# Kernel optimization log

Hardware: AMD Instinct MI355X
Metric: run time of the kernel (lower is better)

The kernel has to match this reference:

```python
import jax, jax.numpy as jnp
import numpy as np

B, T_DEC, T_ENC = 64, 128, 256
D_X, N_HIDDEN, N_FEED = 1024, 1024, 1024


def _glorot(key, shape):
    fan_in = shape[0]
    return jax.random.normal(key, shape, dtype=jnp.float32) / np.sqrt(fan_in)


def setup_inputs() -> dict:
    key = jax.random.key(0)
    ks = jax.random.split(key, 10)
    H = N_HIDDEN
    return {
        "x": jax.random.normal(ks[0], (B, T_DEC, D_X), dtype=jnp.float32),
        "o_enc": jax.random.normal(ks[1], (B, T_ENC, H), dtype=jnp.float32),
        "h_enc": jax.random.normal(ks[2], (B, H), dtype=jnp.float32),
        # input-feeding FFN: Dense(n_feed, tanh), input dim = n_hidden
        "Wfeed": _glorot(ks[3], (H, N_FEED)),
        "bfeed": jnp.zeros((N_FEED,), dtype=jnp.float32),
        # GRU (keras v2, reset_after=True): kernel [n_feed+d_x, 3H], recurrent [H, 3H]
        "Wx": _glorot(ks[4], (N_FEED + D_X, 3 * H)),
        "Wh": _glorot(ks[5], (H, 3 * H)),
        "bxi": jnp.zeros((3 * H,), dtype=jnp.float32),  # input bias
        "bhr": jnp.zeros((3 * H,), dtype=jnp.float32),  # recurrent bias (reset_after)
        # attention FFN: Dense(n_hidden, tanh), input dim = 2H (concat[value, h_dec])
        "Watt": _glorot(ks[6], (2 * H, H)),
        "batt": jnp.zeros((H,), dtype=jnp.float32),
    }


def reference(x, o_enc, h_enc, Wfeed, bfeed, Wx, Wh, bxi, bhr, Watt, batt):
    # x: [B, T_dec, d_x], o_enc: [B, T_enc, H], h_enc: [B, H]
    def step(carry, x_t):
        h, i_feed = carry  # h: [B,H] GRU state, i_feed: [B,H] previous attention output
        # input feeding FFN + concat with current token
        i_cat = jnp.concatenate([jnp.tanh(i_feed @ Wfeed + bfeed), x_t], axis=-1)
        # GRU cell (keras reset_after=True semantics)
        gx = i_cat @ Wx + bxi  # [B, 3H]
        gh = h @ Wh + bhr      # [B, 3H]
        xz, xr, xh = jnp.split(gx, 3, axis=-1)
        hz, hr, hh = jnp.split(gh, 3, axis=-1)
        z = jax.nn.sigmoid(xz + hz)
        r = jax.nn.sigmoid(xr + hr)
        hcand = jnp.tanh(xh + r * hh)
        h_new = z * h + (1.0 - z) * hcand  # [B, H]
        # Luong dot attention over encoder outputs
        scores = jnp.einsum('bh,bth->bt', h_new, o_enc)       # [B, T_enc]
        attn = jax.nn.softmax(scores, axis=-1)
        value = jnp.einsum('bt,bth->bh', attn, o_enc)         # [B, H]
        h_att = jnp.tanh(jnp.concatenate([value, h_new], axis=-1) @ Watt + batt)
        return (h_new, h_att), h_att

    i_feed0 = jnp.zeros_like(h_enc)
    x_t_major = jnp.swapaxes(x, 0, 1)  # [T_dec, B, d_x]
    _, outs = jax.lax.scan(step, (h_enc, i_feed0), x_t_major)
    return jnp.swapaxes(outs, 0, 1)  # [B, T_dec, H]
```

## Files before the change

### kernel.cpp

```cpp
#include <hip/hip_runtime.h>
#include <hip/hip_bf16.h>


#define NWG 256
#define NTHR 1024
constexpr int BB = 64, TD = 128, TE = 256, HH = 1024, H3 = 3072;

typedef __attribute__((ext_vector_type(8))) __bf16 bf16x8;
typedef __attribute__((ext_vector_type(4))) float f32x4;
using bf = __hip_bfloat16;

__device__ __forceinline__ f32x4 mfma16(bf16x8 a, bf16x8 b, f32x4 c) {
  return __builtin_amdgcn_mfma_f32_16x16x32_bf16(a, b, c, 0, 0, 0);
}

struct Args {
  const float *x, *o_enc, *bfeed, *bxi, *bhr, *batt;
  const bf *Wf0, *Wf1, *Wf2, *Wh0, *Wh1, *Wh2;
  const bf *WxF0, *WxF1, *WxF2, *WxX0, *WxX1, *WxX2, *Wa0, *Wa1, *Wa2;
  float *h_f32;
  float *gx;
  float *gh, *scores;
  bf *hs0, *hs1, *hs2, *ff0, *ff1, *ff2, *ifd0, *ifd1, *ifd2;
  bf *xt0, *xt1, *xt2, *vl0, *vl1, *vl2;
  unsigned *cnt, *cnt2, *go, *afl;
  float *out;
};

__device__ __forceinline__ void gbar(unsigned ep, const Args& a, int wg) {
  __syncthreads();
  if (threadIdx.x == 0) {
    __threadfence();
    unsigned* sub = a.cnt + (wg & 15) * 32;
    unsigned o = __hip_atomic_fetch_add(sub, 1u, __ATOMIC_ACQ_REL, __HIP_MEMORY_SCOPE_AGENT);
    if (o == 15) {
      __hip_atomic_store(sub, 0u, __ATOMIC_RELAXED, __HIP_MEMORY_SCOPE_AGENT);
      unsigned o2 = __hip_atomic_fetch_add(a.cnt2, 1u, __ATOMIC_ACQ_REL, __HIP_MEMORY_SCOPE_AGENT);
      if (o2 == 15) {
        __hip_atomic_store(a.cnt2, 0u, __ATOMIC_RELAXED, __HIP_MEMORY_SCOPE_AGENT);
        __hip_atomic_store(a.go, ep, __ATOMIC_RELEASE, __HIP_MEMORY_SCOPE_AGENT);
      }
    }
    while (__hip_atomic_load(a.go, __ATOMIC_RELAXED, __HIP_MEMORY_SCOPE_AGENT) < ep)
      __builtin_amdgcn_s_sleep(2);
    __threadfence();
  }
  __syncthreads();
}

__device__ __forceinline__ void split3_write(bf* p0, bf* p1, bf* p2, size_t i, float v) {
  bf b0 = __float2bfloat16(v);
  float r1 = v - __bfloat162float(b0);
  bf b1 = __float2bfloat16(r1);
  float r2 = r1 - __bfloat162float(b1);
  p0[i] = b0; p1[i] = b1; p2[i] = __float2bfloat16(r2);
}

template <int K>
__device__ __forceinline__ f32x4 gemm6(const bf* A0, const bf* A1, const bf* A2,
                                       const bf* B0, const bf* B1, const bf* B2) {
  f32x4 c0 = {0.f, 0.f, 0.f, 0.f}, c1 = c0, c2 = c0, c3 = c0;
#pragma unroll 4
  for (int k = 0; k < K; k += 32) {
    bf16x8 a0 = *(const bf16x8*)(A0 + k);
    bf16x8 a1 = *(const bf16x8*)(A1 + k);
    bf16x8 a2 = *(const bf16x8*)(A2 + k);
    bf16x8 b0 = *(const bf16x8*)(B0 + k);
    bf16x8 b1 = *(const bf16x8*)(B1 + k);
    bf16x8 b2 = *(const bf16x8*)(B2 + k);
    c0 = mfma16(a0, b0, c0);
    c1 = mfma16(a0, b1, c1);
    c2 = mfma16(a1, b0, c2);
    c3 = mfma16(a1, b1, c3);
    c0 = mfma16(a0, b2, c0);
    c1 = mfma16(a2, b0, c1);
  }
  f32x4 s;
#pragma unroll
  for (int i = 0; i < 4; ++i) s[i] = (c0[i] + c1[i]) + (c2[i] + c3[i]);
  return s;
}

__global__ __launch_bounds__(NTHR, 4) void decoder_main(Args a) {
  const int wg = blockIdx.x;
  const int tid = threadIdx.x;
  const int lane = tid & 63;
  const int wv = tid >> 6;
  const int lrow = lane & 15;
  const int lkg = lane >> 4;

  __shared__ float s_u[4096];
  __shared__ float s_h[HH];
  __shared__ float s_sm[TE];
  __shared__ float s_red[8];
  __shared__ float s_val[2][256];
  __shared__ int s_idx[TE];
  __shared__ int s_wcnt[4];

  unsigned ep = 0;

  for (int t = 0; t < TD; ++t) {
    {
      const bool isf = (wg < 64);
      const int j0 = (isf ? wg : wg - 64) * 16;
      const bf* A0 = isf ? a.ifd0 : a.hs0;
      const bf* A1 = isf ? a.ifd1 : a.hs1;
      const bf* A2 = isf ? a.ifd2 : a.hs2;
      const bf* B0 = isf ? a.Wf0 : a.Wh0;
      const bf* B1 = isf ? a.Wf1 : a.Wh1;
      const bf* B2 = isf ? a.Wf2 : a.Wh2;
      const int mt = wv >> 2, kq = wv & 3;
      const size_t aoff = (size_t)(mt * 16 + lrow) * HH + kq * 256 + lkg * 8;
      const size_t boff = (size_t)(j0 + lrow) * HH + kq * 256 + lkg * 8;
      f32x4 acc = gemm6<256>(A0 + aoff, A1 + aoff, A2 + aoff, B0 + boff, B1 + boff, B2 + boff);
#pragma unroll
      for (int r = 0; r < 4; ++r) s_u[kq * 1024 + mt * 256 + (lkg * 4 + r) * 16 + lrow] = acc[r];
      __syncthreads();
      {
        const int row = tid >> 4, c = tid & 15;
        const int emt = row >> 4, r2 = row & 15;
        const int e = emt * 256 + r2 * 16 + c;
        float v = (s_u[e] + s_u[1024 + e]) + (s_u[2048 + e] + s_u[3072 + e]);
        const int col = j0 + c;
        if (isf) {
          float f = tanhf(v + a.bfeed[col]);
          split3_write(a.ff0, a.ff1, a.ff2, (size_t)row * HH + col, f);
        } else {
          a.gh[(size_t)row * H3 + col] = v + a.bhr[col];
        }
      }
    }
    gbar(++ep, a, wg);

    {
      const int jt = wg >> 2, sub = wg & 3;
      if (wv < 12) {
        const int ci = wv >> 2, ku = wv & 3;
        const int c2 = sub * 3 + ci;
        const int g = c2 >> 2, mt = c2 & 3;
        const int op = ku >> 1, kh = ku & 1;
        const bf* A0 = op ? a.xt0 : a.ff0;
        const bf* A1 = op ? a.xt1 : a.ff1;
        const bf* A2 = op ? a.xt2 : a.ff2;
        const bf* B0 = op ? a.WxX0 : a.WxF0;
        const bf* B1 = op ? a.WxX1 : a.WxF1;
        const bf* B2 = op ? a.WxX2 : a.WxF2;
        const size_t aoff = (size_t)(mt * 16 + lrow) * HH + kh * 512 + lkg * 8;
        const size_t boff = (size_t)(g * HH + jt * 16 + lrow) * HH + kh * 512 + lkg * 8;
        f32x4 acc = gemm6<512>(A0 + aoff, A1 + aoff, A2 + aoff, B0 + boff, B1 + boff, B2 + boff);
#pragma unroll
        for (int r = 0; r < 4; ++r)
          s_u[ci * 1024 + ku * 256 + (lkg * 4 + r) * 16 + lrow] = acc[r];
      }
      __syncthreads();
      if (tid < 768) {
        const int ci2 = tid >> 8, e = tid & 255;
        const int r16 = e >> 4, c16 = e & 15;
        const int base = ci2 * 1024 + e;
        float v = (s_u[base] + s_u[base + 256]) + (s_u[base + 512] + s_u[base + 768]);
        const int c2 = sub * 3 + ci2;
        const int g = c2 >> 2, mt = c2 & 3;
        a.gx[(size_t)(mt * 16 + r16) * H3 + g * 1024 + jt * 16 + c16] = v;
      }
    }
    gbar(++ep, a, wg);

    {
      const int b = wg >> 2, q = wg & 3;
      const float* hold = a.h_f32 + (size_t)(t & 1) * (BB * HH);
      float* hnew = a.h_f32 + (size_t)((t + 1) & 1) * (BB * HH);
      const float* ghb = a.gh + (size_t)b * H3;
      {
        const int col = tid;
        const float* gxb = a.gx + (size_t)b * H3;
        float gz = a.bxi[col] + gxb[col];
        float gr = a.bxi[HH + col] + gxb[HH + col];
        float gc = a.bxi[2 * HH + col] + gxb[2 * HH + col];
        float z = 1.f / (1.f + expf(-(gz + ghb[col])));
        float rr = 1.f / (1.f + expf(-(gr + ghb[HH + col])));
        float hc = tanhf(gc + rr * ghb[2 * HH + col]);
        float hn = z * hold[(size_t)b * HH + col] + (1.f - z) * hc;
        s_h[col] = hn;
        if (q == 0) {
          hnew[(size_t)b * HH + col] = hn;
          split3_write(a.hs0, a.hs1, a.hs2, (size_t)b * HH + col, hn);
        }
      }
      __syncthreads();
      {
        f32x4 sh0 = *(const f32x4*)(s_h + 0 + lane * 4);
        f32x4 sh1 = *(const f32x4*)(s_h + 256 + lane * 4);
        f32x4 sh2 = *(const f32x4*)(s_h + 512 + lane * 4);
        f32x4 sh3 = *(const f32x4*)(s_h + 768 + lane * 4);
        const float* obase = a.o_enc + ((size_t)b * TE + q * 64 + wv * 4) * HH + lane * 4;
        f32x4 o0 = *(const f32x4*)(obase);
        f32x4 o1 = *(const f32x4*)(obase + 256);
        f32x4 o2 = *(const f32x4*)(obase + 512);
        f32x4 o3 = *(const f32x4*)(obase + 768);
#pragma unroll
        for (int i = 0; i < 4; ++i) {
          f32x4 n0, n1, n2, n3;
          if (i + 1 < 4) {
            const float* nr = obase + (size_t)(i + 1) * HH;
            n0 = *(const f32x4*)(nr);
            n1 = *(const f32x4*)(nr + 256);
            n2 = *(const f32x4*)(nr + 512);
            n3 = *(const f32x4*)(nr + 768);
          }
          float s = o0[0] * sh0[0] + o0[1] * sh0[1] + o0[2] * sh0[2] + o0[3] * sh0[3]
                  + o1[0] * sh1[0] + o1[1] * sh1[1] + o1[2] * sh1[2] + o1[3] * sh1[3]
                  + o2[0] * sh2[0] + o2[1] * sh2[1] + o2[2] * sh2[2] + o2[3] * sh2[3]
                  + o3[0] * sh3[0] + o3[1] * sh3[1] + o3[2] * sh3[2] + o3[3] * sh3[3];
          for (int off = 32; off; off >>= 1) s += __shfl_xor(s, off);
          if (lane == 0) a.scores[(size_t)b * TE + q * 64 + wv * 4 + i] = s;
          o0 = n0; o1 = n1; o2 = n2; o3 = n3;
        }
      }
      __syncthreads();
      if (tid == 0) {
        __threadfence();
        __hip_atomic_store(&a.afl[b * 4 + q], (unsigned)(t + 1),
                           __ATOMIC_RELEASE, __HIP_MEMORY_SCOPE_AGENT);
        for (int p = 1; p < 4; ++p) {
          unsigned idx = b * 4 + ((q + p) & 3);
          while (__hip_atomic_load(&a.afl[idx], __ATOMIC_RELAXED, __HIP_MEMORY_SCOPE_AGENT)
                 < (unsigned)(t + 1))
            __builtin_amdgcn_s_sleep(1);
        }
        __threadfence();
      }
      __syncthreads();
      float sc = 0.f, p = 0.f;
      if (tid < 256) {
        sc = a.scores[(size_t)b * TE + tid];
        float v = sc;
        for (int off = 32; off; off >>= 1) v = fmaxf(v, __shfl_xor(v, off));
        if (lane == 0) s_red[wv] = v;
      }
      __syncthreads();
      {
        float mx = fmaxf(fmaxf(s_red[0], s_red[1]), fmaxf(s_red[2], s_red[3]));
        if (tid < 256) {
          p = expf(sc - mx);
          float sum = p;
          for (int off = 32; off; off >>= 1) sum += __shfl_xor(sum, off);
          if (lane == 0) s_red[4 + wv] = sum;
        }
      }
      __syncthreads();
      bool act = false;
      unsigned long long bm = 0;
      if (tid < 256) {
        float tot = s_red[4] + s_red[5] + s_red[6] + s_red[7];
        float w2 = p / tot;
        s_sm[tid] = w2;
        act = (w2 > 1e-8f);
        bm = __ballot(act);
        if (lane == 0) s_wcnt[wv] = __popcll(bm);
      }
      __syncthreads();
      if (tid < 256 && act) {
        int base = 0;
        for (int w2i = 0; w2i < wv; ++w2i) base += s_wcnt[w2i];
        int pos = base + __popcll(bm & ((1ULL << lane) - 1));
        s_idx[pos] = tid;
      }
      __syncthreads();
      const int nact = s_wcnt[0] + s_wcnt[1] + s_wcnt[2] + s_wcnt[3];
      if (tid < 512) {
        const int c = tid & 255, th = tid >> 8;
        const int j = q * 256 + c;
        const float* ob = a.o_enc + (size_t)b * TE * HH + j;
        float accv = 0.f;
        for (int ii = th; ii < nact; ii += 2) {
          const int tt2 = s_idx[ii];
          accv += s_sm[tt2] * ob[(size_t)tt2 * HH];
        }
        s_val[th][c] = accv;
      }
      __syncthreads();
      if (tid < 256)
        split3_write(a.vl0, a.vl1, a.vl2, (size_t)b * HH + q * 256 + tid,
                     s_val[0][tid] + s_val[1][tid]);
    }
    gbar(++ep, a, wg);

    {
      const int cu = wg & 63;
      const int mt = wg >> 6;
      const int kq16 = wv;
      const bool isv = (kq16 < 8);
      const int koff = (kq16 & 7) * 128;
      const bf* A0 = isv ? a.vl0 : a.hs0;
      const bf* A1 = isv ? a.vl1 : a.hs1;
      const bf* A2 = isv ? a.vl2 : a.hs2;
      const size_t aoff = (size_t)(mt * 16 + lrow) * HH + koff + lkg * 8;
      const size_t boff = (size_t)(cu * 16 + lrow) * 2048 + kq16 * 128 + lkg * 8;
      f32x4 acc = gemm6<128>(A0 + aoff, A1 + aoff, A2 + aoff,
                             a.Wa0 + boff, a.Wa1 + boff, a.Wa2 + boff);
#pragma unroll
      for (int r = 0; r < 4; ++r)
        s_u[kq16 * 256 + (lkg * 4 + r) * 16 + lrow] = acc[r];
      __syncthreads();
      if (tid < 256) {
        const int r16 = tid >> 4, c16 = tid & 15;
        const int e = r16 * 16 + c16;
        float v = a.batt[cu * 16 + c16];
#pragma unroll
        for (int kq = 0; kq < 16; ++kq) v += s_u[kq * 256 + e];
        float hv = tanhf(v);
        const int row = mt * 16 + r16;
        const int col = cu * 16 + c16;
        a.out[((size_t)row * TD + t) * HH + col] = hv;
        split3_write(a.ifd0, a.ifd1, a.ifd2, (size_t)row * HH + col, hv);
      }
      if (wg < 64 && t + 1 < TD) {
        split3_write(a.xt0, a.xt1, a.xt2, (size_t)wg * HH + tid,
                     a.x[((size_t)wg * TD + (t + 1)) * HH + tid]);
      }
    }
    gbar(++ep, a, wg);
  }
}

__global__ void k_tr3(const float* src, bf* d0, bf* d1, bf* d2, int R, int C) {
  __shared__ float tile[32][33];
  int c0 = blockIdx.x * 32, r0 = blockIdx.y * 32;
  int tx = threadIdx.x & 31, ty = threadIdx.x >> 5;
  for (int i = ty; i < 32; i += 8)
    tile[i][tx] = src[(size_t)(r0 + i) * C + c0 + tx];
  __syncthreads();
  for (int i = ty; i < 32; i += 8) {
    float v = tile[tx][i];
    size_t o = (size_t)(c0 + i) * R + r0 + tx;
    bf b0 = __float2bfloat16(v);
    float r1 = v - __bfloat162float(b0);
    bf b1 = __float2bfloat16(r1);
    d0[o] = b0; d1[o] = b1; d2[o] = __float2bfloat16(r1 - __bfloat162float(b1));
  }
}

__global__ void k_init(const float* h_enc, float* h_f32, bf* h0, bf* h1, bf* h2,
                       bf* i0, bf* i1, bf* i2, const float* x, bf* x0, bf* x1, bf* x2) {
  int i = blockIdx.x * blockDim.x + threadIdx.x;
  float v = h_enc[i];
  h_f32[i] = v;
  split3_write(h0, h1, h2, i, v);
  bf z = __float2bfloat16(0.f);
  i0[i] = z; i1[i] = z; i2[i] = z;
  int row = i >> 10, col = i & 1023;
  split3_write(x0, x1, x2, i, x[((size_t)row * TD + 0) * HH + col]);
}

extern "C" void kernel_launch(void* const* d_in, const int* in_sizes, int n_in,
                              void* d_out, int out_size, void* d_ws, size_t ws_size,
                              hipStream_t stream) {
  const float* x     = (const float*)d_in[0];
  const float* o_enc = (const float*)d_in[1];
  const float* h_enc = (const float*)d_in[2];
  const float* Wfeed = (const float*)d_in[3];
  const float* bfeed = (const float*)d_in[4];
  const float* Wx    = (const float*)d_in[5];
  const float* Wh    = (const float*)d_in[6];
  const float* bxi   = (const float*)d_in[7];
  const float* bhr   = (const float*)d_in[8];
  const float* Watt  = (const float*)d_in[9];
  const float* batt  = (const float*)d_in[10];

  char* w = (char*)d_ws;
  auto alloc = [&](size_t b) { char* p = w; w += (b + 255) & ~255ULL; return p; };

  const size_t M1 = (size_t)1024 * 1024 * 2;
  bf* Wf[3];  for (auto& p : Wf)  p = (bf*)alloc(M1);
  bf* Wh_[3]; for (auto& p : Wh_) p = (bf*)alloc(3 * M1);
  bf* WxF[3]; for (auto& p : WxF) p = (bf*)alloc(3 * M1);
  bf* WxX[3]; for (auto& p : WxX) p = (bf*)alloc(3 * M1);
  bf* Wa[3];  for (auto& p : Wa)  p = (bf*)alloc(2 * M1);
  float* h_f32  = (float*)alloc((size_t)2 * BB * HH * 4);
  float* gx     = (float*)alloc((size_t)BB * H3 * 4);
  float* gh     = (float*)alloc((size_t)BB * H3 * 4);
  float* scores = (float*)alloc((size_t)BB * TE * 4);
  const size_t AB = (size_t)BB * HH * 2;
  bf *hs[3], *ff[3], *ifd[3], *xt[3], *vl[3];
  for (auto& p : hs)  p = (bf*)alloc(AB);
  for (auto& p : ff)  p = (bf*)alloc(AB);
  for (auto& p : ifd) p = (bf*)alloc(AB);
  for (auto& p : xt)  p = (bf*)alloc(AB);
  for (auto& p : vl)  p = (bf*)alloc(AB);
  unsigned* flags = (unsigned*)alloc(8192);

  hipMemsetAsync(flags, 0, 8192, stream);
  k_tr3<<<dim3(32, 32), 256, 0, stream>>>(Wfeed, Wf[0], Wf[1], Wf[2], 1024, 1024);
  k_tr3<<<dim3(96, 32), 256, 0, stream>>>(Wx, WxF[0], WxF[1], WxF[2], 1024, 3072);
  k_tr3<<<dim3(96, 32), 256, 0, stream>>>(Wx + (size_t)1024 * 3072, WxX[0], WxX[1], WxX[2], 1024, 3072);
  k_tr3<<<dim3(96, 32), 256, 0, stream>>>(Wh, Wh_[0], Wh_[1], Wh_[2], 1024, 3072);
  k_tr3<<<dim3(32, 64), 256, 0, stream>>>(Watt, Wa[0], Wa[1], Wa[2], 2048, 1024);
  k_init<<<BB * HH / 256, 256, 0, stream>>>(h_enc, h_f32, hs[0], hs[1], hs[2],
                                            ifd[0], ifd[1], ifd[2], x, xt[0], xt[1], xt[2]);

  Args a;
  a.x = x; a.o_enc = o_enc; a.bfeed = bfeed; a.bxi = bxi; a.bhr = bhr; a.batt = batt;
  a.Wf0 = Wf[0]; a.Wf1 = Wf[1]; a.Wf2 = Wf[2];
  a.Wh0 = Wh_[0]; a.Wh1 = Wh_[1]; a.Wh2 = Wh_[2];
  a.WxF0 = WxF[0]; a.WxF1 = WxF[1]; a.WxF2 = WxF[2];
  a.WxX0 = WxX[0]; a.WxX1 = WxX[1]; a.WxX2 = WxX[2];
  a.Wa0 = Wa[0]; a.Wa1 = Wa[1]; a.Wa2 = Wa[2];
  a.h_f32 = h_f32; a.gx = gx; a.gh = gh; a.scores = scores;
  a.hs0 = hs[0]; a.hs1 = hs[1]; a.hs2 = hs[2];
  a.ff0 = ff[0]; a.ff1 = ff[1]; a.ff2 = ff[2];
  a.ifd0 = ifd[0]; a.ifd1 = ifd[1]; a.ifd2 = ifd[2];
  a.xt0 = xt[0]; a.xt1 = xt[1]; a.xt2 = xt[2];
  a.vl0 = vl[0]; a.vl1 = vl[1]; a.vl2 = vl[2];
  a.cnt = flags; a.cnt2 = flags + 512; a.go = flags + 544; a.afl = flags + 576;
  a.out = (float*)d_out;

  decoder_main<<<NWG, NTHR, 0, stream>>>(a);
}
```

Baseline: 23.38 ms.

## Remap gx GEMM tiles per workgroup and prefetch next-phase weights into cache

The input-gate GEMM now gives each of 192 workgroups a full 64-row by 16-column tile of one gate, so all 16 waves are busy instead of 12. The attention phase swaps its batch/quarter indexing. Dummy loads are added so that idle or early-finishing workgroups pull the Watt slice and the next step's Wfeed/Wh slices into cache before the phases that read them, hiding global-memory latency behind barriers. The cost is extra memory traffic, and 64 workgroups now sit idle during the gx GEMM.

```diff
diff --git a/kernel.cpp b/kernel.cpp
--- a/kernel.cpp
+++ b/kernel.cpp
@@ -132,13 +132,10 @@
     }
     gbar(++ep, a, wg);
 
-    {
-      const int jt = wg >> 2, sub = wg & 3;
-      if (wv < 12) {
-        const int ci = wv >> 2, ku = wv & 3;
-        const int c2 = sub * 3 + ci;
-        const int g = c2 >> 2, mt = c2 & 3;
-        const int op = ku >> 1, kh = ku & 1;
+    if (wg < 192) {
+      const int jt = wg / 3, g = wg % 3;
+      {
+        const int mt = wv >> 2, op = (wv >> 1) & 1, kh = wv & 1;
         const bf* A0 = op ? a.xt0 : a.ff0;
         const bf* A1 = op ? a.xt1 : a.ff1;
         const bf* A2 = op ? a.xt2 : a.ff2;
@@ -148,25 +145,24 @@
         const size_t aoff = (size_t)(mt * 16 + lrow) * HH + kh * 512 + lkg * 8;
         const size_t boff = (size_t)(g * HH + jt * 16 + lrow) * HH + kh * 512 + lkg * 8;
         f32x4 acc = gemm6<512>(A0 + aoff, A1 + aoff, A2 + aoff, B0 + boff, B1 + boff, B2 + boff);
+        const int s = op * 2 + kh;
 #pragma unroll
         for (int r = 0; r < 4; ++r)
-          s_u[ci * 1024 + ku * 256 + (lkg * 4 + r) * 16 + lrow] = acc[r];
-      }
-      __syncthreads();
-      if (tid < 768) {
-        const int ci2 = tid >> 8, e = tid & 255;
-        const int r16 = e >> 4, c16 = e & 15;
-        const int base = ci2 * 1024 + e;
+          s_u[mt * 1024 + s * 256 + (lkg * 4 + r) * 16 + lrow] = acc[r];
+      }
+      __syncthreads();
+      {
+        const int row = tid >> 4, c16 = tid & 15;
+        const int mt2 = row >> 4, r16 = row & 15;
+        const int base = mt2 * 1024 + r16 * 16 + c16;
         float v = (s_u[base] + s_u[base + 256]) + (s_u[base + 512] + s_u[base + 768]);
-        const int c2 = sub * 3 + ci2;
-        const int g = c2 >> 2, mt = c2 & 3;
-        a.gx[(size_t)(mt * 16 + r16) * H3 + g * 1024 + jt * 16 + c16] = v;
+        a.gx[(size_t)row * H3 + g * 1024 + jt * 16 + c16] = v;
       }
     }
     gbar(++ep, a, wg);
 
     {
-      const int b = wg >> 2, q = wg & 3;
+      const int b = wg & 63, q = wg >> 6;
       const float* hold = a.h_f32 + (size_t)(t & 1) * (BB * HH);
       float* hnew = a.h_f32 + (size_t)((t + 1) & 1) * (BB * HH);
       const float* ghb = a.gh + (size_t)b * H3;
@@ -282,6 +278,21 @@
       if (tid < 256)
         split3_write(a.vl0, a.vl1, a.vl2, (size_t)b * HH + q * 256 + tid,
                      s_val[0][tid] + s_val[1][tid]);
+      if (q == 0) {
+        const size_t wbase = (size_t)(b * 16) * 2048;
+        const char* p0 = (const char*)(a.Wa0 + wbase);
+        const char* p1 = (const char*)(a.Wa1 + wbase);
+        const char* p2 = (const char*)(a.Wa2 + wbase);
+        float sink = 0.f;
+#pragma unroll
+        for (int i = 0; i < 4; ++i) {
+          f32x4 v0 = *(const f32x4*)(p0 + tid * 64 + i * 16);
+          f32x4 v1 = *(const f32x4*)(p1 + tid * 64 + i * 16);
+          f32x4 v2 = *(const f32x4*)(p2 + tid * 64 + i * 16);
+          sink += v0[0] + v1[0] + v2[0];
+        }
+        asm volatile("" :: "v"(sink));
+      }
     }
     gbar(++ep, a, wg);
 
@@ -317,6 +328,22 @@
       if (wg < 64 && t + 1 < TD) {
         split3_write(a.xt0, a.xt1, a.xt2, (size_t)wg * HH + tid,
                      a.x[((size_t)wg * TD + (t + 1)) * HH + tid]);
+      }
+      if (t + 1 < TD) {
+        const bool isf = (wg < 64);
+        const size_t j0p = (size_t)((isf ? wg : wg - 64) * 16) * HH;
+        const char* p0 = (const char*)((isf ? a.Wf0 : a.Wh0) + j0p);
+        const char* p1 = (const char*)((isf ? a.Wf1 : a.Wh1) + j0p);
+        const char* p2 = (const char*)((isf ? a.Wf2 : a.Wh2) + j0p);
+        float sink = 0.f;
+#pragma unroll
+        for (int i = 0; i < 2; ++i) {
+          f32x4 v0 = *(const f32x4*)(p0 + tid * 32 + i * 16);
+          f32x4 v1 = *(const f32x4*)(p1 + tid * 32 + i * 16);
+          f32x4 v2 = *(const f32x4*)(p2 + tid * 32 + i * 16);
+          sink += v0[0] + v1[0] + v2[0];
+        }
+        asm volatile("" :: "v"(sink));
       }
     }
     gbar(++ep, a, wg);
```

After: 25.87 ms. 1.11x slower.
